# Kernel tuning notes

Hardware: AMD Instinct MI355X
Metric: run time of the kernel (lower is better)

Reference implementation:

```python
import jax, jax.numpy as jnp
import numpy as np

D_MODEL, D_STATE, D_CONV, EXPAND = 1024, 16, 4, 2
D_INNER = EXPAND * D_MODEL
B, L = 2, 4096
LN_EPS = 1e-5


def setup_inputs() -> dict:
    key = jax.random.key(0)
    ks = jax.random.split(key, 6)
    x = jax.random.normal(ks[0], (B, L, D_MODEL), dtype=jnp.float32)
    ln_gamma = jnp.ones((D_MODEL,), jnp.float32)
    ln_beta = jnp.zeros((D_MODEL,), jnp.float32)
    W_in = jax.random.normal(ks[1], (2 * D_INNER, D_MODEL), jnp.float32) / np.sqrt(D_MODEL).astype(np.float32)
    conv_w = jax.random.normal(ks[2], (D_INNER, 1, D_CONV), jnp.float32) * 0.1
    conv_b = jnp.zeros((D_INNER,), jnp.float32)
    W_out = jax.random.normal(ks[3], (D_MODEL, D_INNER), jnp.float32) / np.sqrt(D_INNER).astype(np.float32)
    A = jnp.eye(D_STATE, dtype=jnp.float32)
    Bm = jax.random.normal(ks[4], (D_STATE, D_INNER), jnp.float32) * 0.01
    Cm = jax.random.normal(ks[5], (D_STATE, D_INNER), jnp.float32) * 0.01
    return dict(x=x, ln_gamma=ln_gamma, ln_beta=ln_beta, W_in=W_in,
                conv_w=conv_w, conv_b=conv_b, W_out=W_out, A=A, Bm=Bm, Cm=Cm)


def _layernorm(x, gamma, beta):
    mu = jnp.mean(x, axis=-1, keepdims=True)
    var = jnp.mean(jnp.square(x - mu), axis=-1, keepdims=True)
    return (x - mu) * jax.lax.rsqrt(var + LN_EPS) * gamma + beta


def _causal_depthwise_conv(xp, conv_w, conv_b):
    # xp: (B, L, D_INNER) -> torch Conv1d(padding=K-1, groups=C) then slice [:L]
    # == left-pad K-1, valid depthwise conv.
    lhs = jnp.pad(xp.transpose(0, 2, 1), ((0, 0), (0, 0), (D_CONV - 1, 0)))  # (B,C,L+K-1)
    out = jax.lax.conv_general_dilated(
        lhs, conv_w, window_strides=(1,), padding='VALID',
        dimension_numbers=('NCH', 'OIH', 'NCH'), feature_group_count=D_INNER)
    return out.transpose(0, 2, 1) + conv_b  # (B, L, C)


def reference(x, ln_gamma, ln_beta, W_in, conv_w, conv_b, W_out, A, Bm, Cm):
    # scan permutation is identity (untrained optimizer state); masking disabled
    xn = _layernorm(x, ln_gamma, ln_beta)
    xz = jnp.einsum('bld,ed->ble', xn, W_in)          # (B, L, 2*D_INNER)
    x_part, z = jnp.split(xz, 2, axis=-1)             # each (B, L, D_INNER)
    x_conv = jax.nn.silu(_causal_depthwise_conv(x_part, conv_w, conv_b))

    # recurrence: s_t = s_{t-1} @ A.T + u_t @ B.T ; out_t = (x_conv_t + s_t @ C) * sigmoid(z_t)
    u_seq = x_part.transpose(1, 0, 2)                 # (L, B, D_INNER)
    xc_seq = x_conv.transpose(1, 0, 2)
    z_seq = z.transpose(1, 0, 2)

    def step(state, inp):
        u_t, xc_t, z_t = inp
        state = state @ A.T + u_t @ Bm.T              # (B, D_STATE)
        out = (xc_t + state @ Cm) * jax.nn.sigmoid(z_t)
        return state, out

    state0 = jnp.zeros((x.shape[0], D_STATE), x.dtype)
    _, ys = jax.lax.scan(step, state0, (u_seq, xc_seq, z_seq))
    y = ys.transpose(1, 0, 2)                         # (B, L, D_INNER)
    residual = jnp.einsum('bli,di->bld', y, W_out)    # (B, L, D_MODEL)
    return x + residual
```

## Files before the change

kernel.cpp:

```cpp
#include <hip/hip_runtime.h>
#include <hip/hip_bf16.h>
#include <math.h>

#define D_MODEL 1024
#define D_STATE 16
#define D_CONV 4
#define D_INNER 2048
#define BATCH 2
#define SEQ 4096
#define NROW (BATCH * SEQ)
#define LN_EPS 1e-5f

typedef __attribute__((ext_vector_type(8))) short  bf16x8_t;
typedef __attribute__((ext_vector_type(4))) float  f32x4_t;
typedef __attribute__((ext_vector_type(8))) unsigned short u16x8_t;

__device__ inline unsigned short f2bf(float f) {
    unsigned u = __float_as_uint(f);
    u += 0x7fffu + ((u >> 16) & 1u);
    return (unsigned short)(u >> 16);
}
__device__ inline float bf2f(unsigned short u) {
    return __uint_as_float((unsigned)u << 16);
}

#define GLL16(g, l)                                                            \
    __builtin_amdgcn_global_load_lds(                                          \
        (const __attribute__((address_space(1))) void*)(g),                    \
        (__attribute__((address_space(3))) void*)(l), 16, 0, 0)

#define FENCE asm volatile("" ::: "memory")
#define BAR do { FENCE; __builtin_amdgcn_s_barrier(); FENCE; } while (0)

__global__ __launch_bounds__(256) void cvt_bf16(const float* __restrict__ in,
                                                unsigned short* __restrict__ out) {
    const int i = blockIdx.x * 256 + threadIdx.x;
    const float4 a = reinterpret_cast<const float4*>(in)[2 * i];
    const float4 b = reinterpret_cast<const float4*>(in)[2 * i + 1];
    u16x8_t p;
    p[0] = f2bf(a.x); p[1] = f2bf(a.y); p[2] = f2bf(a.z); p[3] = f2bf(a.w);
    p[4] = f2bf(b.x); p[5] = f2bf(b.y); p[6] = f2bf(b.z); p[7] = f2bf(b.w);
    reinterpret_cast<u16x8_t*>(out)[i] = p;
}

__global__ __launch_bounds__(256) void ln_kernel(const float* __restrict__ x,
                                                 const float* __restrict__ gamma,
                                                 const float* __restrict__ beta,
                                                 unsigned short* __restrict__ xn) {
    const int row = blockIdx.x;
    const int tid = threadIdx.x;
    const float4* xr = reinterpret_cast<const float4*>(x + (size_t)row * D_MODEL);
    float4 v = xr[tid];

    __shared__ float red[8];
    const int lane = tid & 63, wave = tid >> 6;

    float s = v.x + v.y + v.z + v.w;
    #pragma unroll
    for (int off = 32; off > 0; off >>= 1) s += __shfl_down(s, off, 64);
    if (lane == 0) red[wave] = s;
    __syncthreads();
    float mu = (red[0] + red[1] + red[2] + red[3]) * (1.0f / D_MODEL);
    __syncthreads();

    float dx = v.x - mu, dy = v.y - mu, dz = v.z - mu, dw = v.w - mu;
    float ss = dx * dx + dy * dy + dz * dz + dw * dw;
    #pragma unroll
    for (int off = 32; off > 0; off >>= 1) ss += __shfl_down(ss, off, 64);
    if (lane == 0) red[wave] = ss;
    __syncthreads();
    float var = (red[0] + red[1] + red[2] + red[3]) * (1.0f / D_MODEL);
    float rs = rsqrtf(var + LN_EPS);

    const float4 gv = reinterpret_cast<const float4*>(gamma)[tid];
    const float4 bv = reinterpret_cast<const float4*>(beta)[tid];
    ushort4 o;
    o.x = f2bf(dx * rs * gv.x + bv.x);
    o.y = f2bf(dy * rs * gv.y + bv.y);
    o.z = f2bf(dz * rs * gv.z + bv.z);
    o.w = f2bf(dw * rs * gv.w + bv.w);
    reinterpret_cast<ushort4*>(xn + (size_t)row * D_MODEL)[tid] = o;
}

__global__ __launch_bounds__(512) void gemm256_bf16(const short* __restrict__ A,
                                                    const short* __restrict__ B,
                                                    unsigned short* __restrict__ Cb,
                                                    int M, int N, int K) {
    __shared__ short lds[2 * 4 * 8192];

    const int tid = threadIdx.x;
    const int w = tid >> 6, l = tid & 63;
    const int row0 = blockIdx.y * 256;
    const int col0 = blockIdx.x * 256;
    const int wm = w >> 2;
    const int wn = w & 3;
    const int fr = l & 15;
    const int fc = (l >> 4) * 8;
    const int NT = K >> 6;

    const int qa = wm;
    const int qb = 2 + (wn >> 1);
    const int bb = (wn & 1) * 64;

    auto STAGE = [&](const short* __restrict__ G, int growbase, int k0,
                     int buf, int q) {
        #pragma unroll
        for (int j = 0; j < 2; ++j) {
            const int e = ((j * 8 + w) << 9) + l * 8;
            const int r = e >> 6;
            const int c = (e & 63) ^ ((r & 7) << 3);
            GLL16(G + (size_t)(growbase + r) * K + k0 + c,
                  &lds[buf * 32768 + q * 8192 + ((j * 8 + w) << 9)]);
        }
    };
    auto LDF = [&](int buf, int q, int r, int ks) -> bf16x8_t {
        const int c = (ks * 32 + fc) ^ ((r & 7) << 3);
        return *reinterpret_cast<const bf16x8_t*>(
            &lds[buf * 32768 + q * 8192 + r * 64 + c]);
    };

    f32x4_t acc[8][4] = {};
    bf16x8_t af[4][2], bA[2][2], bB[2][2];

#define MFMA_Q(mh, nh, bfr)                                                    \
    do {                                                                       \
        _Pragma("unroll")                                                      \
        for (int mi = 0; mi < 4; ++mi)                                         \
            _Pragma("unroll")                                                  \
            for (int ni = 0; ni < 2; ++ni)                                     \
                _Pragma("unroll")                                              \
                for (int ks = 0; ks < 2; ++ks)                                 \
                    acc[(mh) * 4 + mi][(nh) * 2 + ni] =                        \
                        __builtin_amdgcn_mfma_f32_16x16x32_bf16(               \
                            af[mi][ks], bfr[ni][ks],                           \
                            acc[(mh) * 4 + mi][(nh) * 2 + ni], 0, 0, 0);       \
    } while (0)

    STAGE(A, row0,       0, 0, 0);
    STAGE(A, row0 + 128, 0, 0, 1);
    STAGE(B, col0,       0, 0, 2);
    STAGE(B, col0 + 128, 0, 0, 3);
    if (NT > 1) {
        STAGE(B, col0,       64, 1, 2);
        STAGE(B, col0 + 128, 64, 1, 3);
        STAGE(A, row0,       64, 1, 0);
        asm volatile("s_waitcnt vmcnt(6)" ::: "memory");
    } else {
        asm volatile("s_waitcnt vmcnt(0)" ::: "memory");
    }
    BAR;

    for (int kt = 0; kt < NT; ++kt) {
        const int buf = kt & 1, nbuf = buf ^ 1;
        #pragma unroll
        for (int mi = 0; mi < 4; ++mi)
            #pragma unroll
            for (int ks = 0; ks < 2; ++ks)
                af[mi][ks] = LDF(buf, qa, mi * 16 + fr, ks);
        #pragma unroll
        for (int ni = 0; ni < 2; ++ni)
            #pragma unroll
            for (int ks = 0; ks < 2; ++ks)
                bA[ni][ks] = LDF(buf, qb, bb + ni * 16 + fr, ks);
        if (kt + 1 < NT) STAGE(A, row0 + 128, (kt + 1) << 6, nbuf, 1);
        BAR;
        __builtin_amdgcn_s_setprio(1);
        MFMA_Q(0, 0, bA);
        __builtin_amdgcn_s_setprio(0);
        BAR;
        #pragma unroll
        for (int ni = 0; ni < 2; ++ni)
            #pragma unroll
            for (int ks = 0; ks < 2; ++ks)
                bB[ni][ks] = LDF(buf, qb, bb + 32 + ni * 16 + fr, ks);
        BAR;
        __builtin_amdgcn_s_setprio(1);
        MFMA_Q(0, 1, bB);
        __builtin_amdgcn_s_setprio(0);
        BAR;
        #pragma unroll
        for (int mi = 0; mi < 4; ++mi)
            #pragma unroll
            for (int ks = 0; ks < 2; ++ks)
                af[mi][ks] = LDF(buf, qa, 64 + mi * 16 + fr, ks);
        if (kt + 2 < NT) {
            STAGE(B, col0,       (kt + 2) << 6, buf, 2);
            STAGE(B, col0 + 128, (kt + 2) << 6, buf, 3);
        }
        BAR;
        __builtin_amdgcn_s_setprio(1);
        MFMA_Q(1, 1, bB);
        __builtin_amdgcn_s_setprio(0);
        BAR;
        if (kt + 2 < NT) {
            STAGE(A, row0, (kt + 2) << 6, buf, 0);
            asm volatile("s_waitcnt vmcnt(6)" ::: "memory");
        } else {
            asm volatile("s_waitcnt vmcnt(0)" ::: "memory");
        }
        BAR;
        __builtin_amdgcn_s_setprio(1);
        MFMA_Q(1, 0, bA);
        __builtin_amdgcn_s_setprio(0);
        BAR;
    }
#undef MFMA_Q

    const int cr = (l >> 4) * 4;
    const int cc = l & 15;
    #pragma unroll
    for (int m = 0; m < 8; ++m) {
        #pragma unroll
        for (int n = 0; n < 4; ++n) {
            size_t base = (size_t)(row0 + wm * 128 + m * 16 + cr) * N +
                          (col0 + wn * 64 + n * 16 + cc);
            #pragma unroll
            for (int j = 0; j < 4; ++j)
                Cb[base + (size_t)j * N] = f2bf(acc[m][n][j]);
        }
    }
}

__global__ __launch_bounds__(256) void gemm_bf16(const short* __restrict__ A,
                                                 const short* __restrict__ B,
                                                 const float* __restrict__ add,
                                                 float* __restrict__ Cf,
                                                 unsigned short* __restrict__ Cb,
                                                 int M, int N, int K) {
    __shared__ short As[128 * 32];
    __shared__ short Bs[128 * 32];

    const int tid = threadIdx.x;
    const int w = tid >> 6;
    const int l = tid & 63;
    const int row0 = blockIdx.y * 128;
    const int col0 = blockIdx.x * 128;
    const int wr = (w >> 1) * 64;
    const int wc = (w & 1) * 64;

    f32x4_t acc[4][4] = {};

    const int srow = w * 32 + (l >> 2);
    const int scol = ((l & 3) * 8) ^ ((srow & 3) << 3);
    const short* aSrc = A + (size_t)(row0 + srow) * K + scol;
    const short* bSrc = B + (size_t)(col0 + srow) * K + scol;
    const size_t rstep = (size_t)16 * K;

    const int fr = l & 15;
    const int fk0 = (l >> 4) * 8;
    const int fk = fk0 ^ ((fr & 3) << 3);

    for (int k0 = 0; k0 < K; k0 += 32) {
        GLL16(aSrc + k0,         &As[(w * 32) * 32]);
        GLL16(aSrc + k0 + rstep, &As[(w * 32 + 16) * 32]);
        GLL16(bSrc + k0,         &Bs[(w * 32) * 32]);
        GLL16(bSrc + k0 + rstep, &Bs[(w * 32 + 16) * 32]);
        __syncthreads();

        bf16x8_t af[4], bfr[4];
        #pragma unroll
        for (int m = 0; m < 4; ++m)
            af[m] = *reinterpret_cast<const bf16x8_t*>(&As[(wr + m * 16 + fr) * 32 + fk]);
        #pragma unroll
        for (int n = 0; n < 4; ++n)
            bfr[n] = *reinterpret_cast<const bf16x8_t*>(&Bs[(wc + n * 16 + fr) * 32 + fk]);

        #pragma unroll
        for (int m = 0; m < 4; ++m)
            #pragma unroll
            for (int n = 0; n < 4; ++n)
                acc[m][n] = __builtin_amdgcn_mfma_f32_16x16x32_bf16(
                    af[m], bfr[n], acc[m][n], 0, 0, 0);
        __syncthreads();
    }

    const int cr = (l >> 4) * 4;
    const int cc = l & 15;
    #pragma unroll
    for (int m = 0; m < 4; ++m) {
        #pragma unroll
        for (int n = 0; n < 4; ++n) {
            size_t base = (size_t)(row0 + wr + m * 16 + cr) * N + (col0 + wc + n * 16 + cc);
            #pragma unroll
            for (int j = 0; j < 4; ++j) {
                float v = acc[m][n][j];
                if (Cb) {
                    Cb[base + (size_t)j * N] = f2bf(v);
                } else {
                    if (add) v += add[base + (size_t)j * N];
                    Cf[base + (size_t)j * N] = v;
                }
            }
        }
    }
}

__global__ __launch_bounds__(64) void v_mfma(const unsigned short* __restrict__ xz,
                                             const unsigned short* __restrict__ Bmb,
                                             float* __restrict__ V) {
    const int l = threadIdx.x;
    const int r0 = blockIdx.x * 16;
    const int fr = l & 15;
    const int fk = (l >> 4) * 8;

    const unsigned short* aP = xz + (size_t)(r0 + fr) * (2 * D_INNER) + fk;
    const unsigned short* bP = Bmb + fr * D_INNER + fk;

    f32x4_t acc = {};
    #pragma unroll 4
    for (int k0 = 0; k0 < D_INNER; k0 += 32) {
        bf16x8_t a = *reinterpret_cast<const bf16x8_t*>(aP + k0);
        bf16x8_t b = *reinterpret_cast<const bf16x8_t*>(bP + k0);
        acc = __builtin_amdgcn_mfma_f32_16x16x32_bf16(a, b, acc, 0, 0, 0);
    }

    const int cr = (l >> 4) * 4;
    const int cc = l & 15;
    #pragma unroll
    for (int j = 0; j < 4; ++j)
        V[(size_t)(r0 + cr + j) * D_STATE + cc] = acc[j];
}

__global__ __launch_bounds__(256) void check_a(const float* __restrict__ A,
                                               int* __restrict__ flag) {
    const int i = threadIdx.x;
    if (i == 0) *flag = 0;
    __syncthreads();
    const float ex = ((i >> 4) == (i & 15)) ? 1.0f : 0.0f;
    unsigned long long bad = __ballot(A[i] != ex);
    if ((i & 63) == 0 && bad) atomicOr(flag, 1);
}

__global__ __launch_bounds__(256) void scan_par(const float* __restrict__ V,
                                                float* __restrict__ S,
                                                const int* __restrict__ flag) {
    if (*flag) return;
    const int p = blockIdx.x;
    const int b = p >> 4, s = p & 15;
    const int tid = threadIdx.x;
    const float* vb = V + (size_t)b * SEQ * D_STATE + s;
    float* sb = S + (size_t)b * SEQ * D_STATE + s;

    const int t0 = tid * 16;
    float v[16];
    float run = 0.0f;
    #pragma unroll
    for (int j = 0; j < 16; ++j) {
        run += vb[(size_t)(t0 + j) * D_STATE];
        v[j] = run;
    }

    const float tot = run;
    float sc = tot;
    #pragma unroll
    for (int off = 1; off < 64; off <<= 1) {
        float n = __shfl_up(sc, off, 64);
        if ((tid & 63) >= off) sc += n;
    }
    __shared__ float wtot[4];
    if ((tid & 63) == 63) wtot[tid >> 6] = sc;
    __syncthreads();
    float woff = 0.0f;
    #pragma unroll
    for (int w2 = 0; w2 < 4; ++w2)
        if (w2 < (tid >> 6)) woff += wtot[w2];
    const float excl = sc - tot + woff;

    #pragma unroll
    for (int j = 0; j < 16; ++j)
        sb[(size_t)(t0 + j) * D_STATE] = v[j] + excl;
}

#define SCAN_CHUNK 256

__global__ __launch_bounds__(64) void scan_seq(const float* __restrict__ V,
                                               const float* __restrict__ A,
                                               float* __restrict__ S,
                                               const int* __restrict__ flag) {
    if (*flag == 0) return;
    __shared__ float Al[D_STATE * D_STATE];
    __shared__ float Vl[2 * SCAN_CHUNK * D_STATE];
    __shared__ float Sl[2 * SCAN_CHUNK * D_STATE];

    const int tid = threadIdx.x;
    for (int i = tid; i < D_STATE * D_STATE; i += 64) Al[i] = A[i];
    __syncthreads();

    float st = 0.0f;
    const int bb = (tid >> 4) & 1;
    const int ss = tid & 15;

    for (int t0 = 0; t0 < SEQ; t0 += SCAN_CHUNK) {
        for (int idx = tid; idx < 2 * SCAN_CHUNK * D_STATE; idx += 64) {
            int b = idx >> 12;
            int rem = idx & 4095;
            Vl[idx] = V[((size_t)(b * SEQ + t0) * D_STATE) + rem];
        }
        __syncthreads();

        if (tid < 32) {
            float* vb = Vl + bb * SCAN_CHUNK * D_STATE + ss;
            float* sb = Sl + bb * SCAN_CHUNK * D_STATE + ss;
            for (int t = 0; t < SCAN_CHUNK; ++t) {
                float ns = vb[t * D_STATE];
                #pragma unroll
                for (int s2 = 0; s2 < D_STATE; ++s2) {
                    float other = __shfl(st, (tid & 16) | s2, 64);
                    ns = fmaf(Al[ss * D_STATE + s2], other, ns);
                }
                st = ns;
                sb[t * D_STATE] = st;
            }
        }
        __syncthreads();

        for (int idx = tid; idx < 2 * SCAN_CHUNK * D_STATE; idx += 64) {
            int b = idx >> 12;
            int rem = idx & 4095;
            S[((size_t)(b * SEQ + t0) * D_STATE) + rem] = Sl[idx];
        }
        __syncthreads();
    }
}

__global__ __launch_bounds__(256) void y_kernel(const unsigned short* __restrict__ xz,
                                                const float* __restrict__ S,
                                                const float* __restrict__ Cm,
                                                const float* __restrict__ convw,
                                                const float* __restrict__ convb,
                                                unsigned short* __restrict__ y) {
    const int tid = threadIdx.x;
    const int i0 = blockIdx.x * 512 + tid * 2;
    const int r0 = blockIdx.y * 64;
    const int tb0 = r0 & (SEQ - 1);

    const float4 w0 = *reinterpret_cast<const float4*>(&convw[i0 * D_CONV]);
    const float4 w1 = *reinterpret_cast<const float4*>(&convw[(i0 + 1) * D_CONV]);
    const float cb0 = convb[i0], cb1 = convb[i0 + 1];
    float cm0[D_STATE], cm1[D_STATE];
    #pragma unroll
    for (int s = 0; s < D_STATE; ++s) {
        float2 c = *reinterpret_cast<const float2*>(&Cm[s * D_INNER + i0]);
        cm0[s] = c.x; cm1[s] = c.y;
    }

    float2 xm1 = make_float2(0.f, 0.f), xm2 = xm1, xm3 = xm1;
    if (tb0 >= 1) { ushort2 u = *reinterpret_cast<const ushort2*>(&xz[(size_t)(r0 - 1) * (2 * D_INNER) + i0]); xm1 = make_float2(bf2f(u.x), bf2f(u.y)); }
    if (tb0 >= 2) { ushort2 u = *reinterpret_cast<const ushort2*>(&xz[(size_t)(r0 - 2) * (2 * D_INNER) + i0]); xm2 = make_float2(bf2f(u.x), bf2f(u.y)); }
    if (tb0 >= 3) { ushort2 u = *reinterpret_cast<const ushort2*>(&xz[(size_t)(r0 - 3) * (2 * D_INNER) + i0]); xm3 = make_float2(bf2f(u.x), bf2f(u.y)); }

    for (int r = r0; r < r0 + 64; ++r) {
        const ushort2 xu = *reinterpret_cast<const ushort2*>(&xz[(size_t)r * (2 * D_INNER) + i0]);
        const ushort2 zu = *reinterpret_cast<const ushort2*>(&xz[(size_t)r * (2 * D_INNER) + D_INNER + i0]);
        const float2 x0 = make_float2(bf2f(xu.x), bf2f(xu.y));

        float a0 = cb0;
        a0 = fmaf(w0.x, xm3.x, a0); a0 = fmaf(w0.y, xm2.x, a0);
        a0 = fmaf(w0.z, xm1.x, a0); a0 = fmaf(w0.w, x0.x, a0);
        float a1 = cb1;
        a1 = fmaf(w1.x, xm3.y, a1); a1 = fmaf(w1.y, xm2.y, a1);
        a1 = fmaf(w1.z, xm1.y, a1); a1 = fmaf(w1.w, x0.y, a1);

        const float xc0 = a0 / (1.0f + expf(-a0));
        const float xc1 = a1 / (1.0f + expf(-a1));

        const float4* Sp = reinterpret_cast<const float4*>(S + (size_t)r * D_STATE);
        const float4 s0 = Sp[0], s1 = Sp[1], s2 = Sp[2], s3 = Sp[3];
        const float sv[D_STATE] = {s0.x, s0.y, s0.z, s0.w, s1.x, s1.y, s1.z, s1.w,
                                   s2.x, s2.y, s2.z, s2.w, s3.x, s3.y, s3.z, s3.w};
        float sc0 = 0.f, sc1 = 0.f;
        #pragma unroll
        for (int s = 0; s < D_STATE; ++s) {
            sc0 = fmaf(sv[s], cm0[s], sc0);
            sc1 = fmaf(sv[s], cm1[s], sc1);
        }

        const float z0 = bf2f(zu.x), z1 = bf2f(zu.y);
        const float g0 = 1.0f / (1.0f + expf(-z0));
        const float g1 = 1.0f / (1.0f + expf(-z1));

        ushort2 o;
        o.x = f2bf((xc0 + sc0) * g0);
        o.y = f2bf((xc1 + sc1) * g1);
        *reinterpret_cast<ushort2*>(&y[(size_t)r * D_INNER + i0]) = o;

        xm3 = xm2; xm2 = xm1; xm1 = x0;
    }
}

extern "C" void kernel_launch(void* const* d_in, const int* in_sizes, int n_in,
                              void* d_out, int out_size, void* d_ws, size_t ws_size,
                              hipStream_t stream) {
    const float* x      = (const float*)d_in[0];
    const float* ln_g   = (const float*)d_in[1];
    const float* ln_b   = (const float*)d_in[2];
    const float* W_in   = (const float*)d_in[3];
    const float* conv_w = (const float*)d_in[4];
    const float* conv_b = (const float*)d_in[5];
    const float* W_out  = (const float*)d_in[6];
    const float* A      = (const float*)d_in[7];
    const float* Bm     = (const float*)d_in[8];
    const float* Cm     = (const float*)d_in[9];
    float* out = (float*)d_out;

    float* ws = (float*)d_ws;
    float* V  = ws;
    float* S  = V + (size_t)NROW * D_STATE;
    int*   flag = (int*)(S + (size_t)NROW * D_STATE);
    unsigned short* xz_bf  = (unsigned short*)(flag + 64);
    unsigned short* xn_bf  = xz_bf  + (size_t)NROW * 2 * D_INNER;
    unsigned short* Win_bf = xn_bf  + (size_t)NROW * D_MODEL;
    unsigned short* Wout_bf= Win_bf + (size_t)(2 * D_INNER) * D_MODEL;
    unsigned short* y_bf   = Wout_bf + (size_t)D_MODEL * D_INNER;
    unsigned short* Bm_bf  = y_bf   + (size_t)NROW * D_INNER;

    cvt_bf16<<<(2 * D_INNER * D_MODEL) / (256 * 8), 256, 0, stream>>>(W_in, Win_bf);
    cvt_bf16<<<(D_MODEL * D_INNER) / (256 * 8), 256, 0, stream>>>(W_out, Wout_bf);
    cvt_bf16<<<(D_STATE * D_INNER) / (256 * 8), 256, 0, stream>>>(Bm, Bm_bf);

    ln_kernel<<<NROW, 256, 0, stream>>>(x, ln_g, ln_b, xn_bf);

    gemm256_bf16<<<dim3((2 * D_INNER) / 256, NROW / 256), 512, 0, stream>>>(
        (const short*)xn_bf, (const short*)Win_bf, xz_bf,
        NROW, 2 * D_INNER, D_MODEL);

    v_mfma<<<NROW / 16, 64, 0, stream>>>(xz_bf, Bm_bf, V);

    check_a<<<1, 256, 0, stream>>>(A, flag);
    scan_par<<<32, 256, 0, stream>>>(V, S, flag);
    scan_seq<<<1, 64, 0, stream>>>(V, A, S, flag);

    y_kernel<<<dim3(D_INNER / 512, NROW / 64), 256, 0, stream>>>(
        xz_bf, S, Cm, conv_w, conv_b, y_bf);

    gemm_bf16<<<dim3(D_MODEL / 128, NROW / 128), 256, 0, stream>>>(
        (const short*)y_bf, (const short*)Wout_bf, x, out, nullptr,
        NROW, D_MODEL, D_INNER);
}
```

Baseline: 234.2 us.

## Rewrite output GEMM as pipelined 256x128 tile kernel and fuse weight conversions

Replaces the simple single-buffered 128x128 output-projection GEMM with a 512-thread 256x128 tile kernel. It double-buffers LDS through global_load_lds with a K-step of 64 and XOR swizzling, interleaves loads with MFMA phases using barriers and s_setprio, and remaps block IDs for XCD locality. It also merges the three fp32-to-bf16 weight conversion launches into one kernel. The goal is to hide memory latency and cut launch overhead, at the cost of more LDS use, register pressure and barrier count.

```diff
diff --git a/kernel.cpp b/kernel.cpp
--- a/kernel.cpp
+++ b/kernel.cpp
@@ -32,15 +32,25 @@
 #define FENCE asm volatile("" ::: "memory")
 #define BAR do { FENCE; __builtin_amdgcn_s_barrier(); FENCE; } while (0)
 
-__global__ __launch_bounds__(256) void cvt_bf16(const float* __restrict__ in,
-                                                unsigned short* __restrict__ out) {
-    const int i = blockIdx.x * 256 + threadIdx.x;
-    const float4 a = reinterpret_cast<const float4*>(in)[2 * i];
-    const float4 b = reinterpret_cast<const float4*>(in)[2 * i + 1];
+__global__ __launch_bounds__(256) void cvt_all(const float* __restrict__ W_in,
+                                               const float* __restrict__ W_out,
+                                               const float* __restrict__ Bm,
+                                               unsigned short* __restrict__ Win_bf,
+                                               unsigned short* __restrict__ Wout_bf,
+                                               unsigned short* __restrict__ Bm_bf) {
+    const long long g = (long long)(blockIdx.x * 256 + threadIdx.x) * 8;
+    const long long n1 = (long long)2 * D_INNER * D_MODEL;
+    const long long n2 = n1 + (long long)D_MODEL * D_INNER;
+    const float* src; unsigned short* dst; long long off;
+    if (g < n1)      { src = W_in;  dst = Win_bf;  off = g; }
+    else if (g < n2) { src = W_out; dst = Wout_bf; off = g - n1; }
+    else             { src = Bm;    dst = Bm_bf;   off = g - n2; }
+    const float4 a = *reinterpret_cast<const float4*>(src + off);
+    const float4 b = *reinterpret_cast<const float4*>(src + off + 4);
     u16x8_t p;
     p[0] = f2bf(a.x); p[1] = f2bf(a.y); p[2] = f2bf(a.z); p[3] = f2bf(a.w);
     p[4] = f2bf(b.x); p[5] = f2bf(b.y); p[6] = f2bf(b.z); p[7] = f2bf(b.w);
-    reinterpret_cast<u16x8_t*>(out)[i] = p;
+    *reinterpret_cast<u16x8_t*>(dst + off) = p;
 }
 
 __global__ __launch_bounds__(256) void ln_kernel(const float* __restrict__ x,
@@ -221,76 +231,132 @@
     }
 }
 
-__global__ __launch_bounds__(256) void gemm_bf16(const short* __restrict__ A,
-                                                 const short* __restrict__ B,
-                                                 const float* __restrict__ add,
-                                                 float* __restrict__ Cf,
-                                                 unsigned short* __restrict__ Cb,
-                                                 int M, int N, int K) {
-    __shared__ short As[128 * 32];
-    __shared__ short Bs[128 * 32];
+__global__ __launch_bounds__(512) void gemm_out(const short* __restrict__ A,
+                                                const short* __restrict__ B,
+                                                const float* __restrict__ add,
+                                                float* __restrict__ C,
+                                                int M, int N, int K) {
+    __shared__ short lds[2 * 3 * 8192];
 
     const int tid = threadIdx.x;
-    const int w = tid >> 6;
-    const int l = tid & 63;
-    const int row0 = blockIdx.y * 128;
-    const int col0 = blockIdx.x * 128;
-    const int wr = (w >> 1) * 64;
-    const int wc = (w & 1) * 64;
-
-    f32x4_t acc[4][4] = {};
-
-    const int srow = w * 32 + (l >> 2);
-    const int scol = ((l & 3) * 8) ^ ((srow & 3) << 3);
-    const short* aSrc = A + (size_t)(row0 + srow) * K + scol;
-    const short* bSrc = B + (size_t)(col0 + srow) * K + scol;
-    const size_t rstep = (size_t)16 * K;
-
+    const int w = tid >> 6, l = tid & 63;
+
+    const int id = blockIdx.y * gridDim.x + blockIdx.x;
+    const int cpx = (gridDim.x * gridDim.y) >> 3;
+    const int sid = (id & 7) * cpx + (id >> 3);
+    const int row0 = (sid / gridDim.x) * 256;
+    const int col0 = (sid % gridDim.x) * 128;
+
+    const int wm = w >> 2;
+    const int wn = w & 3;
     const int fr = l & 15;
-    const int fk0 = (l >> 4) * 8;
-    const int fk = fk0 ^ ((fr & 3) << 3);
-
-    for (int k0 = 0; k0 < K; k0 += 32) {
-        GLL16(aSrc + k0,         &As[(w * 32) * 32]);
-        GLL16(aSrc + k0 + rstep, &As[(w * 32 + 16) * 32]);
-        GLL16(bSrc + k0,         &Bs[(w * 32) * 32]);
-        GLL16(bSrc + k0 + rstep, &Bs[(w * 32 + 16) * 32]);
-        __syncthreads();
-
-        bf16x8_t af[4], bfr[4];
-        #pragma unroll
-        for (int m = 0; m < 4; ++m)
-            af[m] = *reinterpret_cast<const bf16x8_t*>(&As[(wr + m * 16 + fr) * 32 + fk]);
-        #pragma unroll
-        for (int n = 0; n < 4; ++n)
-            bfr[n] = *reinterpret_cast<const bf16x8_t*>(&Bs[(wc + n * 16 + fr) * 32 + fk]);
-
-        #pragma unroll
-        for (int m = 0; m < 4; ++m)
-            #pragma unroll
-            for (int n = 0; n < 4; ++n)
-                acc[m][n] = __builtin_amdgcn_mfma_f32_16x16x32_bf16(
-                    af[m], bfr[n], acc[m][n], 0, 0, 0);
-        __syncthreads();
-    }
+    const int fc = (l >> 4) * 8;
+    const int NT = K >> 6;
+    const int bb = wn * 32;
+
+    auto STAGE = [&](const short* __restrict__ G, int growbase, int k0,
+                     int buf, int q) {
+        #pragma unroll
+        for (int j = 0; j < 2; ++j) {
+            const int e = ((j * 8 + w) << 9) + l * 8;
+            const int r = e >> 6;
+            const int c = (e & 63) ^ ((r & 7) << 3);
+            GLL16(G + (size_t)(growbase + r) * K + k0 + c,
+                  &lds[buf * 24576 + q * 8192 + ((j * 8 + w) << 9)]);
+        }
+    };
+    auto LDF = [&](int buf, int q, int r, int ks) -> bf16x8_t {
+        const int c = (ks * 32 + fc) ^ ((r & 7) << 3);
+        return *reinterpret_cast<const bf16x8_t*>(
+            &lds[buf * 24576 + q * 8192 + r * 64 + c]);
+    };
+
+    f32x4_t acc[8][2] = {};
+    bf16x8_t af[4][2], bA[2], bB[2];
+
+#define MFMA_H(mh, an, bfr)                                                    \
+    do {                                                                       \
+        _Pragma("unroll")                                                      \
+        for (int mi = 0; mi < 4; ++mi)                                         \
+            _Pragma("unroll")                                                  \
+            for (int ks = 0; ks < 2; ++ks)                                     \
+                acc[(mh) * 4 + mi][(an)] =                                     \
+                    __builtin_amdgcn_mfma_f32_16x16x32_bf16(                   \
+                        af[mi][ks], bfr[ks], acc[(mh) * 4 + mi][(an)], 0, 0, 0);\
+    } while (0)
+
+    STAGE(A, row0,       0, 0, 0);
+    STAGE(A, row0 + 128, 0, 0, 1);
+    STAGE(B, col0,       0, 0, 2);
+    if (NT > 1) {
+        STAGE(B, col0, 64, 1, 2);
+        STAGE(A, row0, 64, 1, 0);
+        asm volatile("s_waitcnt vmcnt(4)" ::: "memory");
+    } else {
+        asm volatile("s_waitcnt vmcnt(0)" ::: "memory");
+    }
+    BAR;
+
+    for (int kt = 0; kt < NT; ++kt) {
+        const int buf = kt & 1, nbuf = buf ^ 1;
+        #pragma unroll
+        for (int mi = 0; mi < 4; ++mi)
+            #pragma unroll
+            for (int ks = 0; ks < 2; ++ks)
+                af[mi][ks] = LDF(buf, wm, mi * 16 + fr, ks);
+        #pragma unroll
+        for (int ks = 0; ks < 2; ++ks)
+            bA[ks] = LDF(buf, 2, bb + fr, ks);
+        if (kt + 1 < NT) STAGE(A, row0 + 128, (kt + 1) << 6, nbuf, 1);
+        BAR;
+        __builtin_amdgcn_s_setprio(1);
+        MFMA_H(0, 0, bA);
+        __builtin_amdgcn_s_setprio(0);
+        BAR;
+        #pragma unroll
+        for (int ks = 0; ks < 2; ++ks)
+            bB[ks] = LDF(buf, 2, bb + 16 + fr, ks);
+        BAR;
+        __builtin_amdgcn_s_setprio(1);
+        MFMA_H(0, 1, bB);
+        __builtin_amdgcn_s_setprio(0);
+        BAR;
+        #pragma unroll
+        for (int mi = 0; mi < 4; ++mi)
+            #pragma unroll
+            for (int ks = 0; ks < 2; ++ks)
+                af[mi][ks] = LDF(buf, wm, 64 + mi * 16 + fr, ks);
+        if (kt + 2 < NT) STAGE(B, col0, (kt + 2) << 6, buf, 2);
+        BAR;
+        __builtin_amdgcn_s_setprio(1);
+        MFMA_H(1, 1, bB);
+        __builtin_amdgcn_s_setprio(0);
+        BAR;
+        if (kt + 2 < NT) {
+            STAGE(A, row0, (kt + 2) << 6, buf, 0);
+            asm volatile("s_waitcnt vmcnt(4)" ::: "memory");
+        } else {
+            asm volatile("s_waitcnt vmcnt(0)" ::: "memory");
+        }
+        BAR;
+        __builtin_amdgcn_s_setprio(1);
+        MFMA_H(1, 0, bA);
+        __builtin_amdgcn_s_setprio(0);
+        BAR;
+    }
+#undef MFMA_H
 
     const int cr = (l >> 4) * 4;
     const int cc = l & 15;
     #pragma unroll
-    for (int m = 0; m < 4; ++m) {
-        #pragma unroll
-        for (int n = 0; n < 4; ++n) {
-            size_t base = (size_t)(row0 + wr + m * 16 + cr) * N + (col0 + wc + n * 16 + cc);
-            #pragma unroll
-            for (int j = 0; j < 4; ++j) {
-                float v = acc[m][n][j];
-                if (Cb) {
-                    Cb[base + (size_t)j * N] = f2bf(v);
-                } else {
-                    if (add) v += add[base + (size_t)j * N];
-                    Cf[base + (size_t)j * N] = v;
-                }
-            }
+    for (int m = 0; m < 8; ++m) {
+        #pragma unroll
+        for (int n = 0; n < 2; ++n) {
+            size_t base = (size_t)(row0 + wm * 128 + m * 16 + cr) * N +
+                          (col0 + wn * 32 + n * 16 + cc);
+            #pragma unroll
+            for (int j = 0; j < 4; ++j)
+                C[base + (size_t)j * N] = acc[m][n][j] + add[base + (size_t)j * N];
         }
     }
 }
@@ -511,12 +577,10 @@
     unsigned short* xn_bf  = xz_bf  + (size_t)NROW * 2 * D_INNER;
     unsigned short* Win_bf = xn_bf  + (size_t)NROW * D_MODEL;
     unsigned short* Wout_bf= Win_bf + (size_t)(2 * D_INNER) * D_MODEL;
-    unsigned short* y_bf   = Wout_bf + (size_t)D_MODEL * D_INNER;
-    unsigned short* Bm_bf  = y_bf   + (size_t)NROW * D_INNER;
-
-    cvt_bf16<<<(2 * D_INNER * D_MODEL) / (256 * 8), 256, 0, stream>>>(W_in, Win_bf);
-    cvt_bf16<<<(D_MODEL * D_INNER) / (256 * 8), 256, 0, stream>>>(W_out, Wout_bf);
-    cvt_bf16<<<(D_STATE * D_INNER) / (256 * 8), 256, 0, stream>>>(Bm, Bm_bf);
+    unsigned short* Bm_bf  = Wout_bf + (size_t)D_MODEL * D_INNER;
+    unsigned short* y_bf   = Bm_bf  + (size_t)D_STATE * D_INNER;
+
+    cvt_all<<<3088, 256, 0, stream>>>(W_in, W_out, Bm, Win_bf, Wout_bf, Bm_bf);
 
     ln_kernel<<<NROW, 256, 0, stream>>>(x, ln_g, ln_b, xn_bf);
 
@@ -533,7 +597,7 @@
     y_kernel<<<dim3(D_INNER / 512, NROW / 64), 256, 0, stream>>>(
         xz_bf, S, Cm, conv_w, conv_b, y_bf);
 
-    gemm_bf16<<<dim3(D_MODEL / 128, NROW / 128), 256, 0, stream>>>(
-        (const short*)y_bf, (const short*)Wout_bf, x, out, nullptr,
+    gemm_out<<<dim3(D_MODEL / 128, NROW / 256), 512, 0, stream>>>(
+        (const short*)y_bf, (const short*)Wout_bf, x, out,
         NROW, D_MODEL, D_INNER);
 }
```

New measurement: 203.2 us. 13.2% less time.
